# Performance work log

Hardware: AMD Instinct MI355X
Metric: run time of the kernel (lower is better)

The kernel has to match this reference:

```python
import jax, jax.numpy as jnp
import numpy as np

EPS = 1e-12  # F.normalize eps


def _gather_nb(var, idx):
    # var: [B, N, C], idx: [B, N, K] -> [B, N, K, C]; out[b,n,k,c] = var[b, idx[b,n,k], c]
    return jnp.take_along_axis(var[:, :, None, :], idx[:, :, :, None], axis=1)


def _l2norm(v):
    n = jnp.sqrt(jnp.sum(v * v, axis=-1, keepdims=True))
    return v / jnp.maximum(n, EPS)


def setup_inputs() -> dict:
    key = jax.random.key(0)
    ks = jax.random.split(key, 16)
    B, N, K, dim, hid = 4, 4096, 16, 128, 64
    s = 0.05
    return {
        "pos": jax.random.normal(ks[0], (B, N, 3), jnp.float32),
        "x": jax.random.normal(ks[1], (B, dim, N), jnp.float32),
        "idx": jax.random.randint(ks[2], (B, N, K), 0, N, jnp.int64),
        "dist": jax.random.uniform(ks[3], (B, N, K), jnp.float32),
        "W_qkv": jax.random.normal(ks[4], (3 * dim, dim), jnp.float32) * s,
        "W1": jax.random.normal(ks[5], (hid, 10), jnp.float32) * s,
        "b1": jax.random.normal(ks[6], (hid,), jnp.float32) * s,
        "W2": jax.random.normal(ks[7], (dim, hid), jnp.float32) * s,
        "b2": jax.random.normal(ks[8], (dim,), jnp.float32) * s,
        "Wm1": jax.random.normal(ks[9], (4 * dim, dim), jnp.float32) * s,
        "bm1": jax.random.normal(ks[10], (4 * dim,), jnp.float32) * s,
        "Wm2": jax.random.normal(ks[11], (dim, 4 * dim), jnp.float32) * s,
        "bm2": jax.random.normal(ks[12], (dim,), jnp.float32) * s,
    }


def reference(pos, x, idx, dist, W_qkv, W1, b1, W2, b2, Wm1, bm1, Wm2, bm2):
    B, _, N = x.shape
    xt = jnp.transpose(x, (0, 2, 1))                      # [B, N, C]
    qkv = xt @ W_qkv.T                                    # [B, N, 3C]
    Q, K_, V = jnp.split(qkv, 3, axis=-1)

    Qg = _gather_nb(Q, idx)                               # [B, N, K, C]
    Kg = _gather_nb(K_, idx)
    Vg = _gather_nb(V, idx)

    # position embedding: [center(3) | neighbor(3) | diff(3) | dist(1)] -> MLP 10->hid->C
    pos_nb = _gather_nb(pos, idx)                         # [B, N, K, 3]
    pos_c = jnp.broadcast_to(pos[:, :, None, :], pos_nb.shape)
    feat10 = jnp.concatenate(
        [pos_c, pos_nb, pos_c - pos_nb, dist[..., None]], axis=-1)  # [B, N, K, 10]
    pos_emb = jax.nn.relu(feat10 @ W1.T + b1) @ W2.T + b2  # [B, N, K, C]

    Knorm = _l2norm(Kg + pos_emb)                         # [B, N, K, C]
    Vrel = jax.nn.relu(Vg + pos_emb)                      # [B, N, K, C]
    Qn = _l2norm(Qg)                                      # [B, N, K, C]

    # kv_context: contract over N per neighbor slot k -> [B, K, C, C]
    kv = jnp.einsum('bnkc,bnkd->bkcd', Knorm, Vrel)
    # (1/N) Qn @ kv, then sum over k -> [B, N, C]
    agg = jnp.einsum('bnkc,bkcd->bnd', Qn, kv) / N

    out = jax.nn.relu(agg @ Wm1.T + bm1) @ Wm2.T + bm2 + xt  # [B, N, C]
    return jnp.transpose(out, (0, 2, 1))                     # [B, C, N]
```

## Files before the change

### kernel.cpp

```cpp
#include <hip/hip_runtime.h>
#include <math.h>

#define Bn 4
#define Nn 4096
#define Kn 16
#define Cn 128
#define HIDn 64

#define OFF_WQKVBF 0
#define OFF_WM1BF  24576
#define OFF_WM2BF  57344
#define OFF_W2BFG  90112
#define OFF_W1PBF  94208
#define OFF_QNBF   95232
#define OFF_KMBF   1143808
#define OFF_VMBF   2192384
#define OFF_KVT32  3240960
#define OFF_KVTBF  4289536
#define OFF_AGG0   4813824
#define OFF_AGG1   6910976
#define OFF_FLAG   9008128

typedef short bf16x8 __attribute__((ext_vector_type(8)));
typedef float f32x4 __attribute__((ext_vector_type(4)));

__device__ inline unsigned short f2bf(float f) {
  union { float f; unsigned u; } v; v.f = f;
  unsigned r = v.u + 0x7fffu + ((v.u >> 16) & 1u);
  return (unsigned short)(r >> 16);
}
__device__ inline float b2f(unsigned short s) {
  union { unsigned u; float f; } v; v.u = ((unsigned)s) << 16; return v.f;
}

__global__ void k0_prep(const float* __restrict__ Wqkv,
                        const float* __restrict__ Wm1, const float* __restrict__ Wm2,
                        const float* __restrict__ W2, const float* __restrict__ W1,
                        const int* __restrict__ idx_raw, float* ws) {
  if (blockIdx.x == 0 && threadIdx.x == 0) {
    int any = 0;
    for (int i = 0; i < 64; ++i) any |= idx_raw[2 * i + 1];
    ((int*)(ws + OFF_FLAG))[0] = (any == 0) ? 1 : 0;
  }
  int t = blockIdx.x * 256 + threadIdx.x;
  if (t < 49152) { ((unsigned short*)(ws + OFF_WQKVBF))[t] = f2bf(Wqkv[t]); return; }
  t -= 49152;
  if (t < 65536) { ((unsigned short*)(ws + OFF_WM1BF))[t] = f2bf(Wm1[t]); return; }
  t -= 65536;
  if (t < 65536) { ((unsigned short*)(ws + OFF_WM2BF))[t] = f2bf(Wm2[t]); return; }
  t -= 65536;
  if (t < 8192) { ((unsigned short*)(ws + OFF_W2BFG))[t] = f2bf(W2[t]); return; }
  t -= 8192;
  if (t < 2048) {
    int o = t >> 5, i = t & 31;
    ((unsigned short*)(ws + OFF_W1PBF))[t] = (i < 10) ? f2bf(W1[o * 10 + i]) : 0;
    return;
  }
}

__global__ __launch_bounds__(256, 2) void k1_qkv(const float* __restrict__ x, float* ws) {
  __shared__ __align__(16) unsigned short a_lds[32 * 136];
  __shared__ __align__(16) float qkv_lds[32 * 388];
  const unsigned short* Wq = (const unsigned short*)(ws + OFF_WQKVBF);
  unsigned short* Qnbf = (unsigned short*)(ws + OFF_QNBF);
  unsigned short* KmBF = (unsigned short*)(ws + OFF_KMBF);
  unsigned short* VmBF = (unsigned short*)(ws + OFF_VMBF);
  int b = blockIdx.x >> 7;
  int n0 = (blockIdx.x & 127) << 5;
  int t = threadIdx.x;
  int w = t >> 6, l = t & 63, ml = l & 15, gq = l >> 4;
#pragma unroll
  for (int i = 0; i < 16; ++i) {
    int id = t + 256 * i;
    int c = id >> 5, j = id & 31;
    a_lds[j * 136 + c] = f2bf(x[(b * Cn + c) * Nn + n0 + j]);
  }
  __syncthreads();
  f32x4 acc[2][6];
#pragma unroll
  for (int i = 0; i < 2; ++i)
#pragma unroll
    for (int j = 0; j < 6; ++j) acc[i][j] = (f32x4)0.f;
#pragma unroll
  for (int kc = 0; kc < 4; ++kc) {
    bf16x8 av0 = *(const bf16x8*)&a_lds[ml * 136 + kc * 32 + 8 * gq];
    bf16x8 av1 = *(const bf16x8*)&a_lds[(ml + 16) * 136 + kc * 32 + 8 * gq];
#pragma unroll
    for (int nf = 0; nf < 6; ++nf) {
      int m = 96 * w + 16 * nf + ml;
      bf16x8 bv = *(const bf16x8*)&Wq[m * 128 + kc * 32 + 8 * gq];
      acc[0][nf] = __builtin_amdgcn_mfma_f32_16x16x32_bf16(av0, bv, acc[0][nf], 0, 0, 0);
      acc[1][nf] = __builtin_amdgcn_mfma_f32_16x16x32_bf16(av1, bv, acc[1][nf], 0, 0, 0);
    }
  }
#pragma unroll
  for (int mf = 0; mf < 2; ++mf)
#pragma unroll
    for (int nf = 0; nf < 6; ++nf)
#pragma unroll
      for (int r = 0; r < 4; ++r)
        qkv_lds[(16 * mf + 4 * gq + r) * 388 + 96 * w + 16 * nf + ml] = acc[mf][nf][r];
  __syncthreads();
  {
    int g = t >> 3, l8 = t & 7;
    float4 q4[4];
    float ss = 0.f;
#pragma unroll
    for (int q = 0; q < 4; ++q) {
      q4[q] = *(const float4*)&qkv_lds[g * 388 + l8 * 16 + 4 * q];
      ss = fmaf(q4[q].x, q4[q].x, ss); ss = fmaf(q4[q].y, q4[q].y, ss);
      ss = fmaf(q4[q].z, q4[q].z, ss); ss = fmaf(q4[q].w, q4[q].w, ss);
    }
    ss += __shfl_xor(ss, 1); ss += __shfl_xor(ss, 2); ss += __shfl_xor(ss, 4);
    float sc = 1.f / fmaxf(sqrtf(ss), 1e-12f);
    union { unsigned short us[8]; uint4 u4; } o0, o1;
#pragma unroll
    for (int q = 0; q < 2; ++q) {
      o0.us[q * 4 + 0] = f2bf(q4[q].x * sc); o0.us[q * 4 + 1] = f2bf(q4[q].y * sc);
      o0.us[q * 4 + 2] = f2bf(q4[q].z * sc); o0.us[q * 4 + 3] = f2bf(q4[q].w * sc);
    }
#pragma unroll
    for (int q = 0; q < 2; ++q) {
      o1.us[q * 4 + 0] = f2bf(q4[2 + q].x * sc); o1.us[q * 4 + 1] = f2bf(q4[2 + q].y * sc);
      o1.us[q * 4 + 2] = f2bf(q4[2 + q].z * sc); o1.us[q * 4 + 3] = f2bf(q4[2 + q].w * sc);
    }
    *(uint4*)&Qnbf[(b * Nn + n0 + g) * Cn + l8 * 16] = o0.u4;
    *(uint4*)&Qnbf[(b * Nn + n0 + g) * Cn + l8 * 16 + 8] = o1.u4;
  }
#pragma unroll
  for (int i = 0; i < 2; ++i) {
    int id = t + 256 * i;
    int row = id >> 4, c8 = id & 15;
    const float* kp = &qkv_lds[row * 388 + 128 + c8 * 8];
    const float* vp = &qkv_lds[row * 388 + 256 + c8 * 8];
    union { unsigned short us[8]; uint4 u4; } ko, vo;
#pragma unroll
    for (int j = 0; j < 8; ++j) { ko.us[j] = f2bf(kp[j]); vo.us[j] = f2bf(vp[j]); }
    *(uint4*)&KmBF[(b * Nn + n0 + row) * Cn + c8 * 8] = ko.u4;
    *(uint4*)&VmBF[(b * Nn + n0 + row) * Cn + c8 * 8] = vo.u4;
  }
}

#define CH2 8
__global__ __launch_bounds__(256, 3) void k2_kv(const float* __restrict__ pos,
                                                const float* __restrict__ dist,
                                                const int* __restrict__ idxp,
                                                const float* __restrict__ b1,
                                                const float* __restrict__ b2,
                                                float* ws) {
  __shared__ __align__(16) unsigned short feat[32 * 40];
  __shared__ __align__(16) unsigned short h_lds[32 * 72];
  __shared__ __align__(16) unsigned short pe_bf[32 * 136];
  __shared__ __align__(16) unsigned short K_rm[32 * 136];
  __shared__ __align__(16) unsigned short V_rm[32 * 136];
  __shared__ __align__(16) unsigned short KnT[128 * 40];
  __shared__ __align__(16) unsigned short VrT[128 * 40];

  const unsigned short* KmBF = (const unsigned short*)(ws + OFF_KMBF);
  const unsigned short* VmBF = (const unsigned short*)(ws + OFF_VMBF);
  const unsigned short* W2g = (const unsigned short*)(ws + OFF_W2BFG);
  const unsigned short* W1P = (const unsigned short*)(ws + OFF_W1PBF);
  float* kvt = ws + OFF_KVT32;
  int flag = ((const int*)(ws + OFF_FLAG))[0];

  int bid = blockIdx.x;
  int b = bid & 3;
  int rest = bid >> 2;
  int k = rest & 15, ch = rest >> 4;
  int t = threadIdx.x;
  int w = t >> 6, l = t & 63;
  int ml = l & 15, gq = l >> 4;

  int nl = (t >> 3) & 7, half = t & 7;
  int n_b2 = 8 * w + nl;
  int side = t >> 7, cc = t & 127;
  bool is32 = (t < 32);

  float b1v = b1[16 * w + ml];
  float b2v0 = b2[32 * w + ml];
  float b2v1 = b2[32 * w + 16 + ml];

  f32x4 acc[2][8];
#pragma unroll
  for (int i = 0; i < 2; ++i)
#pragma unroll
    for (int j = 0; j < 8; ++j) acc[i][j] = (f32x4)0.f;

  int nbase = ch * 512;
  union U8 { unsigned short us[8]; uint4 u4; };

  float dd = 0.f, pc0 = 0.f, pc1 = 0.f, pc2 = 0.f, pn0 = 0.f, pn1 = 0.f, pn2 = 0.f;
  if (is32) {
    int fidx_m = (b * Nn + nbase + t) * Kn + k;
    int jn_m = flag ? idxp[2 * fidx_m] : idxp[fidx_m];
    dd = dist[fidx_m];
    pc0 = pos[(b * Nn + nbase + t) * 3 + 0];
    pc1 = pos[(b * Nn + nbase + t) * 3 + 1];
    pc2 = pos[(b * Nn + nbase + t) * 3 + 2];
    pn0 = pos[(b * Nn + jn_m) * 3 + 0];
    pn1 = pos[(b * Nn + jn_m) * 3 + 1];
    pn2 = pos[(b * Nn + jn_m) * 3 + 2];
  }
  int fidx_b = (b * Nn + nbase + n_b2) * Kn + k;
  int jn_b = flag ? idxp[2 * fidx_b] : idxp[fidx_b];
  U8 ka, kb, va, vb;
  {
    const unsigned short* krow = &KmBF[(b * Nn + jn_b) * Cn];
    const unsigned short* vrow = &VmBF[(b * Nn + jn_b) * Cn];
    ka.u4 = *(const uint4*)&krow[half * 16];
    kb.u4 = *(const uint4*)&krow[half * 16 + 8];
    va.u4 = *(const uint4*)&vrow[half * 16];
    vb.u4 = *(const uint4*)&vrow[half * 16 + 8];
  }
  if (is32) {
    float f10[10] = {pc0, pc1, pc2, pn0, pn1, pn2, pc0 - pn0, pc1 - pn1, pc2 - pn2, dd};
    U8 f0, f1, z;
#pragma unroll
    for (int j = 0; j < 8; ++j) f0.us[j] = f2bf(f10[j]);
    f1.us[0] = f2bf(f10[8]); f1.us[1] = f2bf(f10[9]);
#pragma unroll
    for (int j = 2; j < 8; ++j) f1.us[j] = 0;
#pragma unroll
    for (int j = 0; j < 8; ++j) z.us[j] = 0;
    *(uint4*)&feat[t * 40] = f0.u4;
    *(uint4*)&feat[t * 40 + 8] = f1.u4;
    *(uint4*)&feat[t * 40 + 16] = z.u4;
    *(uint4*)&feat[t * 40 + 24] = z.u4;
  }

  for (int it = 0; it < 16; ++it) {
    __syncthreads();
    {
      bf16x8 fa0 = *(const bf16x8*)&feat[ml * 40 + 8 * gq];
      bf16x8 fa1 = *(const bf16x8*)&feat[(ml + 16) * 40 + 8 * gq];
      bf16x8 wv = *(const bf16x8*)&W1P[(16 * w + ml) * 32 + 8 * gq];
      f32x4 h0 = (f32x4)0.f, h1 = (f32x4)0.f;
      h0 = __builtin_amdgcn_mfma_f32_16x16x32_bf16(fa0, wv, h0, 0, 0, 0);
      h1 = __builtin_amdgcn_mfma_f32_16x16x32_bf16(fa1, wv, h1, 0, 0, 0);
#pragma unroll
      for (int r = 0; r < 4; ++r) {
        h_lds[(4 * gq + r) * 72 + 16 * w + ml] = f2bf(fmaxf(h0[r] + b1v, 0.f));
        h_lds[(16 + 4 * gq + r) * 72 + 16 * w + ml] = f2bf(fmaxf(h1[r] + b1v, 0.f));
      }
    }
    int itn = (it < 15) ? it + 1 : 15;
    int n0n = nbase + itn * 32;
    int jn_mn = 0;
    float ddn = 0.f;
    if (is32) {
      int fidx_mn = (b * Nn + n0n + t) * Kn + k;
      jn_mn = flag ? idxp[2 * fidx_mn] : idxp[fidx_mn];
      ddn = dist[fidx_mn];
    }
    int fidx_bn = (b * Nn + n0n + n_b2) * Kn + k;
    int jn_bn = flag ? idxp[2 * fidx_bn] : idxp[fidx_bn];
    __syncthreads();
    {
      f32x4 pacc[2][2];
#pragma unroll
      for (int i = 0; i < 2; ++i)
#pragma unroll
        for (int j = 0; j < 2; ++j) pacc[i][j] = (f32x4)0.f;
#pragma unroll
      for (int hc = 0; hc < 64; hc += 32) {
        bf16x8 av[2];
#pragma unroll
        for (int mf = 0; mf < 2; ++mf)
          av[mf] = *(const bf16x8*)&h_lds[(ml + 16 * mf) * 72 + hc + 8 * gq];
#pragma unroll
        for (int nf = 0; nf < 2; ++nf) {
          int c = 32 * w + 16 * nf + ml;
          bf16x8 bv = *(const bf16x8*)&W2g[c * 64 + hc + 8 * gq];
          pacc[0][nf] = __builtin_amdgcn_mfma_f32_16x16x32_bf16(av[0], bv, pacc[0][nf], 0, 0, 0);
          pacc[1][nf] = __builtin_amdgcn_mfma_f32_16x16x32_bf16(av[1], bv, pacc[1][nf], 0, 0, 0);
        }
      }
#pragma unroll
      for (int mf = 0; mf < 2; ++mf)
#pragma unroll
        for (int nf = 0; nf < 2; ++nf) {
          int c = 32 * w + 16 * nf + ml;
          float bias = nf ? b2v1 : b2v0;
#pragma unroll
          for (int r = 0; r < 4; ++r)
            pe_bf[(16 * mf + 4 * gq + r) * 136 + c] = f2bf(pacc[mf][nf][r] + bias);
        }
    }
    __syncthreads();
    {
      U8 pa, pb;
      pa.u4 = *(const uint4*)&pe_bf[n_b2 * 136 + half * 16];
      pb.u4 = *(const uint4*)&pe_bf[n_b2 * 136 + half * 16 + 8];
      float kr[16], vr[16];
      float ss = 0.f;
#pragma unroll
      for (int j = 0; j < 16; ++j) {
        float pe = b2f((j < 8) ? pa.us[j] : pb.us[j - 8]);
        float kg = b2f((j < 8) ? ka.us[j] : kb.us[j - 8]);
        float vg = b2f((j < 8) ? va.us[j] : vb.us[j - 8]);
        kr[j] = kg + pe;
        vr[j] = fmaxf(vg + pe, 0.f);
        ss = fmaf(kr[j], kr[j], ss);
      }
      ss += __shfl_xor(ss, 1); ss += __shfl_xor(ss, 2); ss += __shfl_xor(ss, 4);
      float sc = 1.f / fmaxf(sqrtf(ss), 1e-12f);
      union { unsigned short us[8]; uint4 u4; } o;
#pragma unroll
      for (int hh = 0; hh < 2; ++hh) {
#pragma unroll
        for (int j = 0; j < 8; ++j) o.us[j] = f2bf(kr[hh * 8 + j] * sc);
        *(uint4*)&K_rm[n_b2 * 136 + half * 16 + 8 * hh] = o.u4;
      }
#pragma unroll
      for (int hh = 0; hh < 2; ++hh) {
#pragma unroll
        for (int j = 0; j < 8; ++j) o.us[j] = f2bf(vr[hh * 8 + j]);
        *(uint4*)&V_rm[n_b2 * 136 + half * 16 + 8 * hh] = o.u4;
      }
    }
    float pc0n = 0.f, pc1n = 0.f, pc2n = 0.f, pn0n = 0.f, pn1n = 0.f, pn2n = 0.f;
    if (is32) {
      pc0n = pos[(b * Nn + n0n + t) * 3 + 0];
      pc1n = pos[(b * Nn + n0n + t) * 3 + 1];
      pc2n = pos[(b * Nn + n0n + t) * 3 + 2];
      pn0n = pos[(b * Nn + jn_mn) * 3 + 0];
      pn1n = pos[(b * Nn + jn_mn) * 3 + 1];
      pn2n = pos[(b * Nn + jn_mn) * 3 + 2];
    }
    U8 kan, kbn, van, vbn;
    {
      const unsigned short* krow = &KmBF[(b * Nn + jn_bn) * Cn];
      const unsigned short* vrow = &VmBF[(b * Nn + jn_bn) * Cn];
      kan.u4 = *(const uint4*)&krow[half * 16];
      kbn.u4 = *(const uint4*)&krow[half * 16 + 8];
      van.u4 = *(const uint4*)&vrow[half * 16];
      vbn.u4 = *(const uint4*)&vrow[half * 16 + 8];
    }
    __syncthreads();
    {
      const unsigned short* src = side ? V_rm : K_rm;
      unsigned short* dst = side ? VrT : KnT;
      unsigned v[16];
#pragma unroll
      for (int i = 0; i < 16; ++i) {
        unsigned lo = src[(2 * i) * 136 + cc];
        unsigned hi = src[(2 * i + 1) * 136 + cc];
        v[i] = lo | (hi << 16);
      }
#pragma unroll
      for (int i = 0; i < 4; ++i) {
        uint4 pk = {v[4 * i], v[4 * i + 1], v[4 * i + 2], v[4 * i + 3]};
        *(uint4*)&dst[cc * 40 + 8 * i] = pk;
      }
    }
    __syncthreads();
    {
      bf16x8 av[2];
#pragma unroll
      for (int mf = 0; mf < 2; ++mf)
        av[mf] = *(const bf16x8*)&VrT[(32 * w + 16 * mf + ml) * 40 + 8 * gq];
#pragma unroll
      for (int nf = 0; nf < 8; ++nf) {
        bf16x8 bv = *(const bf16x8*)&KnT[(16 * nf + ml) * 40 + 8 * gq];
#pragma unroll
        for (int mf = 0; mf < 2; ++mf)
          acc[mf][nf] = __builtin_amdgcn_mfma_f32_16x16x32_bf16(av[mf], bv, acc[mf][nf], 0, 0, 0);
      }
    }
    if (is32) {
      float f10[10] = {pc0n, pc1n, pc2n, pn0n, pn1n, pn2n,
                       pc0n - pn0n, pc1n - pn1n, pc2n - pn2n, ddn};
      U8 f0, f1, z;
#pragma unroll
      for (int j = 0; j < 8; ++j) f0.us[j] = f2bf(f10[j]);
      f1.us[0] = f2bf(f10[8]); f1.us[1] = f2bf(f10[9]);
#pragma unroll
      for (int j = 2; j < 8; ++j) f1.us[j] = 0;
#pragma unroll
      for (int j = 0; j < 8; ++j) z.us[j] = 0;
      *(uint4*)&feat[t * 40] = f0.u4;
      *(uint4*)&feat[t * 40 + 8] = f1.u4;
      *(uint4*)&feat[t * 40 + 16] = z.u4;
      *(uint4*)&feat[t * 40 + 24] = z.u4;
    }
    ka.u4 = kan.u4; kb.u4 = kbn.u4; va.u4 = van.u4; vb.u4 = vbn.u4;
  }
  float* kvp = kvt + (b * Kn + k) * Cn * Cn;
#pragma unroll
  for (int mf = 0; mf < 2; ++mf)
#pragma unroll
    for (int nf = 0; nf < 8; ++nf) {
      int c = 16 * nf + ml;
#pragma unroll
      for (int r = 0; r < 4; ++r) {
        int d = 32 * w + 16 * mf + 4 * gq + r;
        atomicAdd(&kvp[d * Cn + c], acc[mf][nf][r]);
      }
    }
}

__global__ __launch_bounds__(256) void k2b_cvt(float* ws) {
  const float* src = ws + OFF_KVT32;
  unsigned short* dst = (unsigned short*)(ws + OFF_KVTBF);
  int i = blockIdx.x * 256 + threadIdx.x;
  float4 a = *(const float4*)&src[i * 8];
  float4 c = *(const float4*)&src[i * 8 + 4];
  union { unsigned short us[8]; uint4 u4; } o;
  o.us[0] = f2bf(a.x); o.us[1] = f2bf(a.y); o.us[2] = f2bf(a.z); o.us[3] = f2bf(a.w);
  o.us[4] = f2bf(c.x); o.us[5] = f2bf(c.y); o.us[6] = f2bf(c.z); o.us[7] = f2bf(c.w);
  *(uint4*)&dst[i * 8] = o.u4;
}

__global__ __launch_bounds__(256, 4) void k3_agg(const int* __restrict__ idxp, float* ws) {
  __shared__ __align__(16) unsigned short qt[32 * 136];
  const unsigned short* Qnbf = (const unsigned short*)(ws + OFF_QNBF);
  const unsigned short* kvtbf = (const unsigned short*)(ws + OFF_KVTBF);
  int flag = ((const int*)(ws + OFF_FLAG))[0];

  int bid = blockIdx.x;
  int b = bid & 3;
  int kh = (bid >> 2) & 1;
  int nt = bid >> 3;
  int n0 = nt * 32;
  int t = threadIdx.x;
  int w = t >> 6, l = t & 63;
  int ml = l & 15, gq = l >> 4;

  f32x4 acc[2][2];
#pragma unroll
  for (int i = 0; i < 2; ++i)
#pragma unroll
    for (int j = 0; j < 2; ++j) acc[i][j] = (f32x4)0.f;

  for (int kk = 0; kk < 8; ++kk) {
    int k = kh * 8 + kk;
    __syncthreads();
#pragma unroll
    for (int i = 0; i < 2; ++i) {
      int id = t + 256 * i;
      int row = id >> 4, c16 = id & 15;
      int fidx = (b * Nn + n0 + row) * Kn + k;
      int jn = flag ? idxp[2 * fidx] : idxp[fidx];
      uint4 v = *(const uint4*)&Qnbf[(b * Nn + jn) * Cn + c16 * 8];
      *(uint4*)&qt[row * 136 + c16 * 8] = v;
    }
    __syncthreads();
    const unsigned short* kvp = &kvtbf[(b * Kn + k) * Cn * Cn];
#pragma unroll
    for (int c0 = 0; c0 < 128; c0 += 32) {
      bf16x8 a0 = *(const bf16x8*)&qt[ml * 136 + c0 + 8 * gq];
      bf16x8 a1 = *(const bf16x8*)&qt[(ml + 16) * 136 + c0 + 8 * gq];
#pragma unroll
      for (int nf = 0; nf < 2; ++nf) {
        int d = 32 * w + 16 * nf + ml;
        bf16x8 bv = *(const bf16x8*)&kvp[d * Cn + c0 + 8 * gq];
        acc[0][nf] = __builtin_amdgcn_mfma_f32_16x16x32_bf16(a0, bv, acc[0][nf], 0, 0, 0);
        acc[1][nf] = __builtin_amdgcn_mfma_f32_16x16x32_bf16(a1, bv, acc[1][nf], 0, 0, 0);
      }
    }
  }
  float* ag = ws + (kh ? OFF_AGG1 : OFF_AGG0);
#pragma unroll
  for (int mf = 0; mf < 2; ++mf)
#pragma unroll
    for (int nf = 0; nf < 2; ++nf) {
      int d = 32 * w + 16 * nf + ml;
#pragma unroll
      for (int r = 0; r < 4; ++r) {
        int n = n0 + 16 * mf + 4 * gq + r;
        ag[(b * Nn + n) * Cn + d] = acc[mf][nf][r];
      }
    }
}

__global__ __launch_bounds__(256, 2) void k4_mlp(const float* __restrict__ x,
                                                 const float* __restrict__ bm1,
                                                 const float* __restrict__ bm2,
                                                 float* __restrict__ out, float* ws) {
  __shared__ __align__(16) unsigned short a_lds[32 * 136];
  __shared__ __align__(16) unsigned short h_lds[32 * 520];
  __shared__ float out_s[128 * 33];
  const float* agg0 = ws + OFF_AGG0;
  const float* agg1 = ws + OFF_AGG1;
  const unsigned short* Wm1bf = (const unsigned short*)(ws + OFF_WM1BF);
  const unsigned short* Wm2bf = (const unsigned short*)(ws + OFF_WM2BF);
  const float invN = 1.f / (float)Nn;
  int b = blockIdx.x >> 7;
  int n0 = (blockIdx.x & 127) << 5;
  int t = threadIdx.x;
  int w = t >> 6, l = t & 63, ml = l & 15, gq = l >> 4;
#pragma unroll
  for (int i = 0; i < 4; ++i) {
    int id = t + 256 * i;
    int row = id >> 5, c4 = id & 31;
    int off = (b * Nn + n0 + row) * Cn + c4 * 4;
    float4 v0 = *(const float4*)&agg0[off];
    float4 v1 = *(const float4*)&agg1[off];
    union { unsigned short us[4]; uint2 u2; } o;
    o.us[0] = f2bf((v0.x + v1.x) * invN); o.us[1] = f2bf((v0.y + v1.y) * invN);
    o.us[2] = f2bf((v0.z + v1.z) * invN); o.us[3] = f2bf((v0.w + v1.w) * invN);
    *(uint2*)&a_lds[row * 136 + c4 * 4] = o.u2;
  }
  __syncthreads();
  {
    f32x4 hacc[2][8];
#pragma unroll
    for (int i = 0; i < 2; ++i)
#pragma unroll
      for (int j = 0; j < 8; ++j) hacc[i][j] = (f32x4)0.f;
#pragma unroll
    for (int kc = 0; kc < 4; ++kc) {
      bf16x8 av0 = *(const bf16x8*)&a_lds[ml * 136 + kc * 32 + 8 * gq];
      bf16x8 av1 = *(const bf16x8*)&a_lds[(ml + 16) * 136 + kc * 32 + 8 * gq];
#pragma unroll
      for (int nf = 0; nf < 8; ++nf) {
        int h = 128 * w + 16 * nf + ml;
        bf16x8 bv = *(const bf16x8*)&Wm1bf[h * 128 + kc * 32 + 8 * gq];
        hacc[0][nf] = __builtin_amdgcn_mfma_f32_16x16x32_bf16(av0, bv, hacc[0][nf], 0, 0, 0);
        hacc[1][nf] = __builtin_amdgcn_mfma_f32_16x16x32_bf16(av1, bv, hacc[1][nf], 0, 0, 0);
      }
    }
#pragma unroll
    for (int mf = 0; mf < 2; ++mf)
#pragma unroll
      for (int nf = 0; nf < 8; ++nf) {
        int h = 128 * w + 16 * nf + ml;
        float bias = bm1[h];
#pragma unroll
        for (int r = 0; r < 4; ++r)
          h_lds[(16 * mf + 4 * gq + r) * 520 + h] = f2bf(fmaxf(hacc[mf][nf][r] + bias, 0.f));
      }
  }
  __syncthreads();
  {
    f32x4 oacc[2][2];
#pragma unroll
    for (int i = 0; i < 2; ++i)
#pragma unroll
      for (int j = 0; j < 2; ++j) oacc[i][j] = (f32x4)0.f;
#pragma unroll
    for (int kc = 0; kc < 16; ++kc) {
      bf16x8 av0 = *(const bf16x8*)&h_lds[ml * 520 + kc * 32 + 8 * gq];
      bf16x8 av1 = *(const bf16x8*)&h_lds[(ml + 16) * 520 + kc * 32 + 8 * gq];
#pragma unroll
      for (int nf = 0; nf < 2; ++nf) {
        int co = 32 * w + 16 * nf + ml;
        bf16x8 bv = *(const bf16x8*)&Wm2bf[co * 512 + kc * 32 + 8 * gq];
        oacc[0][nf] = __builtin_amdgcn_mfma_f32_16x16x32_bf16(av0, bv, oacc[0][nf], 0, 0, 0);
        oacc[1][nf] = __builtin_amdgcn_mfma_f32_16x16x32_bf16(av1, bv, oacc[1][nf], 0, 0, 0);
      }
    }
#pragma unroll
    for (int mf = 0; mf < 2; ++mf)
#pragma unroll
      for (int nf = 0; nf < 2; ++nf) {
        int co = 32 * w + 16 * nf + ml;
        float bias = bm2[co];
#pragma unroll
        for (int r = 0; r < 4; ++r)
          out_s[co * 33 + 16 * mf + 4 * gq + r] = oacc[mf][nf][r] + bias;
      }
  }
  __syncthreads();
#pragma unroll
  for (int i = 0; i < 16; ++i) {
    int id = t + 256 * i;
    int co = id >> 5, j = id & 31;
    out[(b * Cn + co) * Nn + n0 + j] = out_s[co * 33 + j] + x[(b * Cn + co) * Nn + n0 + j];
  }
}

extern "C" void kernel_launch(void* const* d_in, const int* in_sizes, int n_in,
                              void* d_out, int out_size, void* d_ws, size_t ws_size,
                              hipStream_t stream) {
  const float* pos  = (const float*)d_in[0];
  const float* x    = (const float*)d_in[1];
  const int*   idx  = (const int*)d_in[2];
  const float* dist = (const float*)d_in[3];
  const float* Wqkv = (const float*)d_in[4];
  const float* W1   = (const float*)d_in[5];
  const float* b1   = (const float*)d_in[6];
  const float* W2   = (const float*)d_in[7];
  const float* b2   = (const float*)d_in[8];
  const float* Wm1  = (const float*)d_in[9];
  const float* bm1  = (const float*)d_in[10];
  const float* Wm2  = (const float*)d_in[11];
  const float* bm2  = (const float*)d_in[12];
  float* out = (float*)d_out;
  float* ws = (float*)d_ws;

  hipMemsetAsync(ws + OFF_KVT32, 0, (size_t)Bn * Kn * Cn * Cn * sizeof(float), stream);
  hipLaunchKernelGGL(k0_prep, dim3(744), dim3(256), 0, stream, Wqkv, Wm1, Wm2, W2, W1, idx, ws);
  hipLaunchKernelGGL(k1_qkv, dim3(Bn * 128), dim3(256), 0, stream, x, ws);
  hipLaunchKernelGGL(k2_kv, dim3(Bn * Kn * CH2), dim3(256), 0, stream, pos, dist, idx, b1, b2, ws);
  hipLaunchKernelGGL(k2b_cvt, dim3(512), dim3(256), 0, stream, ws);
  hipLaunchKernelGGL(k3_agg, dim3(Bn * 2 * 128), dim3(256), 0, stream, idx, ws);
  hipLaunchKernelGGL(k4_mlp, dim3(Bn * 128), dim3(256), 0, stream, x, bm1, bm2, out, ws);
}
```

Baseline: 172.3 us.

## Fuse pos-MLP epilogue with K/V gather and write transposed tiles directly

After: 315.2 us. 1.83x slower.

```diff
diff --git a/kernel.cpp b/kernel.cpp
--- a/kernel.cpp
+++ b/kernel.cpp
@@ -141,8 +141,8 @@
   }
 }
 
-#define CH2 8
-__global__ __launch_bounds__(256, 3) void k2_kv(const float* __restrict__ pos,
+#define CH2 16
+__global__ __launch_bounds__(256, 4) void k2_kv(const float* __restrict__ pos,
                                                 const float* __restrict__ dist,
                                                 const int* __restrict__ idxp,
                                                 const float* __restrict__ b1,
@@ -150,9 +150,6 @@
                                                 float* ws) {
   __shared__ __align__(16) unsigned short feat[32 * 40];
   __shared__ __align__(16) unsigned short h_lds[32 * 72];
-  __shared__ __align__(16) unsigned short pe_bf[32 * 136];
-  __shared__ __align__(16) unsigned short K_rm[32 * 136];
-  __shared__ __align__(16) unsigned short V_rm[32 * 136];
   __shared__ __align__(16) unsigned short KnT[128 * 40];
   __shared__ __align__(16) unsigned short VrT[128 * 40];
 
@@ -170,15 +167,15 @@
   int t = threadIdx.x;
   int w = t >> 6, l = t & 63;
   int ml = l & 15, gq = l >> 4;
-
-  int nl = (t >> 3) & 7, half = t & 7;
-  int n_b2 = 8 * w + nl;
-  int side = t >> 7, cc = t & 127;
+  int nhalf = w & 1;
+  bool isV = (w >= 2);
   bool is32 = (t < 32);
+  const unsigned short* Grow = isV ? VmBF : KmBF;
 
   float b1v = b1[16 * w + ml];
-  float b2v0 = b2[32 * w + ml];
-  float b2v1 = b2[32 * w + 16 + ml];
+  float b2v[8];
+#pragma unroll
+  for (int nf = 0; nf < 8; ++nf) b2v[nf] = b2[16 * nf + ml];
 
   f32x4 acc[2][8];
 #pragma unroll
@@ -186,9 +183,14 @@
 #pragma unroll
     for (int j = 0; j < 8; ++j) acc[i][j] = (f32x4)0.f;
 
-  int nbase = ch * 512;
-  union U8 { unsigned short us[8]; uint4 u4; };
-
+  int nbase = ch * 256;
+
+  int jn_g[4];
+#pragma unroll
+  for (int r = 0; r < 4; ++r) {
+    int fidx = (b * Nn + nbase + 16 * nhalf + 4 * gq + r) * Kn + k;
+    jn_g[r] = flag ? idxp[2 * fidx] : idxp[fidx];
+  }
   float dd = 0.f, pc0 = 0.f, pc1 = 0.f, pc2 = 0.f, pn0 = 0.f, pn1 = 0.f, pn2 = 0.f;
   if (is32) {
     int fidx_m = (b * Nn + nbase + t) * Kn + k;
@@ -200,21 +202,8 @@
     pn0 = pos[(b * Nn + jn_m) * 3 + 0];
     pn1 = pos[(b * Nn + jn_m) * 3 + 1];
     pn2 = pos[(b * Nn + jn_m) * 3 + 2];
-  }
-  int fidx_b = (b * Nn + nbase + n_b2) * Kn + k;
-  int jn_b = flag ? idxp[2 * fidx_b] : idxp[fidx_b];
-  U8 ka, kb, va, vb;
-  {
-    const unsigned short* krow = &KmBF[(b * Nn + jn_b) * Cn];
-    const unsigned short* vrow = &VmBF[(b * Nn + jn_b) * Cn];
-    ka.u4 = *(const uint4*)&krow[half * 16];
-    kb.u4 = *(const uint4*)&krow[half * 16 + 8];
-    va.u4 = *(const uint4*)&vrow[half * 16];
-    vb.u4 = *(const uint4*)&vrow[half * 16 + 8];
-  }
-  if (is32) {
     float f10[10] = {pc0, pc1, pc2, pn0, pn1, pn2, pc0 - pn0, pc1 - pn1, pc2 - pn2, dd};
-    U8 f0, f1, z;
+    union { unsigned short us[8]; uint4 u4; } f0, f1, z;
 #pragma unroll
     for (int j = 0; j < 8; ++j) f0.us[j] = f2bf(f10[j]);
     f1.us[0] = f2bf(f10[8]); f1.us[1] = f2bf(f10[9]);
@@ -228,7 +217,7 @@
     *(uint4*)&feat[t * 40 + 24] = z.u4;
   }
 
-  for (int it = 0; it < 16; ++it) {
+  for (int it = 0; it < 8; ++it) {
     __syncthreads();
     {
       bf16x8 fa0 = *(const bf16x8*)&feat[ml * 40 + 8 * gq];
@@ -243,8 +232,21 @@
         h_lds[(16 + 4 * gq + r) * 72 + 16 * w + ml] = f2bf(fmaxf(h1[r] + b1v, 0.f));
       }
     }
-    int itn = (it < 15) ? it + 1 : 15;
+    unsigned short rowg[8][4];
+#pragma unroll
+    for (int r = 0; r < 4; ++r) {
+      const unsigned short* base = &Grow[(b * Nn + jn_g[r]) * Cn + ml];
+#pragma unroll
+      for (int nf = 0; nf < 8; ++nf) rowg[nf][r] = base[16 * nf];
+    }
+    int itn = (it < 7) ? it + 1 : 7;
     int n0n = nbase + itn * 32;
+    int jn_gn[4];
+#pragma unroll
+    for (int r = 0; r < 4; ++r) {
+      int fidx = (b * Nn + n0n + 16 * nhalf + 4 * gq + r) * Kn + k;
+      jn_gn[r] = flag ? idxp[2 * fidx] : idxp[fidx];
+    }
     int jn_mn = 0;
     float ddn = 0.f;
     if (is32) {
@@ -252,70 +254,54 @@
       jn_mn = flag ? idxp[2 * fidx_mn] : idxp[fidx_mn];
       ddn = dist[fidx_mn];
     }
-    int fidx_bn = (b * Nn + n0n + n_b2) * Kn + k;
-    int jn_bn = flag ? idxp[2 * fidx_bn] : idxp[fidx_bn];
     __syncthreads();
     {
-      f32x4 pacc[2][2];
-#pragma unroll
-      for (int i = 0; i < 2; ++i)
-#pragma unroll
-        for (int j = 0; j < 2; ++j) pacc[i][j] = (f32x4)0.f;
-#pragma unroll
-      for (int hc = 0; hc < 64; hc += 32) {
-        bf16x8 av[2];
-#pragma unroll
-        for (int mf = 0; mf < 2; ++mf)
-          av[mf] = *(const bf16x8*)&h_lds[(ml + 16 * mf) * 72 + hc + 8 * gq];
-#pragma unroll
-        for (int nf = 0; nf < 2; ++nf) {
-          int c = 32 * w + 16 * nf + ml;
-          bf16x8 bv = *(const bf16x8*)&W2g[c * 64 + hc + 8 * gq];
-          pacc[0][nf] = __builtin_amdgcn_mfma_f32_16x16x32_bf16(av[0], bv, pacc[0][nf], 0, 0, 0);
-          pacc[1][nf] = __builtin_amdgcn_mfma_f32_16x16x32_bf16(av[1], bv, pacc[1][nf], 0, 0, 0);
+      bf16x8 av0 = *(const bf16x8*)&h_lds[(16 * nhalf + ml) * 72 + 8 * gq];
+      bf16x8 av1 = *(const bf16x8*)&h_lds[(16 * nhalf + ml) * 72 + 32 + 8 * gq];
+      float ss[4] = {0.f, 0.f, 0.f, 0.f};
+      unsigned kp[8][2];
+#pragma unroll
+      for (int nf = 0; nf < 8; ++nf) {
+        bf16x8 bv0 = *(const bf16x8*)&W2g[(16 * nf + ml) * 64 + 8 * gq];
+        bf16x8 bv1 = *(const bf16x8*)&W2g[(16 * nf + ml) * 64 + 32 + 8 * gq];
+        f32x4 p = (f32x4)0.f;
+        p = __builtin_amdgcn_mfma_f32_16x16x32_bf16(av0, bv0, p, 0, 0, 0);
+        p = __builtin_amdgcn_mfma_f32_16x16x32_bf16(av1, bv1, p, 0, 0, 0);
+        if (!isV) {
+          float v0 = b2f(rowg[nf][0]) + p[0] + b2v[nf];
+          float v1 = b2f(rowg[nf][1]) + p[1] + b2v[nf];
+          float v2 = b2f(rowg[nf][2]) + p[2] + b2v[nf];
+          float v3 = b2f(rowg[nf][3]) + p[3] + b2v[nf];
+          ss[0] = fmaf(v0, v0, ss[0]); ss[1] = fmaf(v1, v1, ss[1]);
+          ss[2] = fmaf(v2, v2, ss[2]); ss[3] = fmaf(v3, v3, ss[3]);
+          kp[nf][0] = (unsigned)f2bf(v0) | ((unsigned)f2bf(v1) << 16);
+          kp[nf][1] = (unsigned)f2bf(v2) | ((unsigned)f2bf(v3) << 16);
+        } else {
+#pragma unroll
+          for (int r = 0; r < 4; ++r) {
+            float vv = fmaxf(b2f(rowg[nf][r]) + p[r] + b2v[nf], 0.f);
+            VrT[(16 * nf + ml) * 40 + 16 * nhalf + 4 * gq + r] = f2bf(vv);
+          }
         }
       }
-#pragma unroll
-      for (int mf = 0; mf < 2; ++mf)
-#pragma unroll
-        for (int nf = 0; nf < 2; ++nf) {
-          int c = 32 * w + 16 * nf + ml;
-          float bias = nf ? b2v1 : b2v0;
-#pragma unroll
-          for (int r = 0; r < 4; ++r)
-            pe_bf[(16 * mf + 4 * gq + r) * 136 + c] = f2bf(pacc[mf][nf][r] + bias);
+      if (!isV) {
+        float sc[4];
+#pragma unroll
+        for (int r = 0; r < 4; ++r) {
+          float s = ss[r];
+          s += __shfl_xor(s, 1); s += __shfl_xor(s, 2);
+          s += __shfl_xor(s, 4); s += __shfl_xor(s, 8);
+          sc[r] = 1.f / fmaxf(sqrtf(s), 1e-12f);
         }
-    }
-    __syncthreads();
-    {
-      U8 pa, pb;
-      pa.u4 = *(const uint4*)&pe_bf[n_b2 * 136 + half * 16];
-      pb.u4 = *(const uint4*)&pe_bf[n_b2 * 136 + half * 16 + 8];
-      float kr[16], vr[16];
-      float ss = 0.f;
-#pragma unroll
-      for (int j = 0; j < 16; ++j) {
-        float pe = b2f((j < 8) ? pa.us[j] : pb.us[j - 8]);
-        float kg = b2f((j < 8) ? ka.us[j] : kb.us[j - 8]);
-        float vg = b2f((j < 8) ? va.us[j] : vb.us[j - 8]);
-        kr[j] = kg + pe;
-        vr[j] = fmaxf(vg + pe, 0.f);
-        ss = fmaf(kr[j], kr[j], ss);
-      }
-      ss += __shfl_xor(ss, 1); ss += __shfl_xor(ss, 2); ss += __shfl_xor(ss, 4);
-      float sc = 1.f / fmaxf(sqrtf(ss), 1e-12f);
-      union { unsigned short us[8]; uint4 u4; } o;
-#pragma unroll
-      for (int hh = 0; hh < 2; ++hh) {
-#pragma unroll
-        for (int j = 0; j < 8; ++j) o.us[j] = f2bf(kr[hh * 8 + j] * sc);
-        *(uint4*)&K_rm[n_b2 * 136 + half * 16 + 8 * hh] = o.u4;
-      }
-#pragma unroll
-      for (int hh = 0; hh < 2; ++hh) {
-#pragma unroll
-        for (int j = 0; j < 8; ++j) o.us[j] = f2bf(vr[hh * 8 + j]);
-        *(uint4*)&V_rm[n_b2 * 136 + half * 16 + 8 * hh] = o.u4;
+#pragma unroll
+        for (int nf = 0; nf < 8; ++nf) {
+#pragma unroll
+          for (int r = 0; r < 4; ++r) {
+            unsigned bits = (r & 1) ? (kp[nf][r >> 1] >> 16) : (kp[nf][r >> 1] & 0xffffu);
+            float val = b2f((unsigned short)bits) * sc[r];
+            KnT[(16 * nf + ml) * 40 + 16 * nhalf + 4 * gq + r] = f2bf(val);
+          }
+        }
       }
     }
     float pc0n = 0.f, pc1n = 0.f, pc2n = 0.f, pn0n = 0.f, pn1n = 0.f, pn2n = 0.f;
@@ -327,50 +313,24 @@
       pn1n = pos[(b * Nn + jn_mn) * 3 + 1];
       pn2n = pos[(b * Nn + jn_mn) * 3 + 2];
     }
-    U8 kan, kbn, van, vbn;
-    {
-      const unsigned short* krow = &KmBF[(b * Nn + jn_bn) * Cn];
-      const unsigned short* vrow = &VmBF[(b * Nn + jn_bn) * Cn];
-      kan.u4 = *(const uint4*)&krow[half * 16];
-      kbn.u4 = *(const uint4*)&krow[half * 16 + 8];
-      van.u4 = *(const uint4*)&vrow[half * 16];
-      vbn.u4 = *(const uint4*)&vrow[half * 16 + 8];
-    }
     __syncthreads();
     {
-      const unsigned short* src = side ? V_rm : K_rm;
-      unsigned short* dst = side ? VrT : KnT;
-      unsigned v[16];
-#pragma unroll
-      for (int i = 0; i < 16; ++i) {
-        unsigned lo = src[(2 * i) * 136 + cc];
-        unsigned hi = src[(2 * i + 1) * 136 + cc];
-        v[i] = lo | (hi << 16);
-      }
-#pragma unroll
-      for (int i = 0; i < 4; ++i) {
-        uint4 pk = {v[4 * i], v[4 * i + 1], v[4 * i + 2], v[4 * i + 3]};
-        *(uint4*)&dst[cc * 40 + 8 * i] = pk;
-      }
-    }
-    __syncthreads();
-    {
-      bf16x8 av[2];
+      bf16x8 avv[2];
 #pragma unroll
       for (int mf = 0; mf < 2; ++mf)
-        av[mf] = *(const bf16x8*)&VrT[(32 * w + 16 * mf + ml) * 40 + 8 * gq];
+        avv[mf] = *(const bf16x8*)&VrT[(32 * w + 16 * mf + ml) * 40 + 8 * gq];
 #pragma unroll
       for (int nf = 0; nf < 8; ++nf) {
         bf16x8 bv = *(const bf16x8*)&KnT[(16 * nf + ml) * 40 + 8 * gq];
 #pragma unroll
         for (int mf = 0; mf < 2; ++mf)
-          acc[mf][nf] = __builtin_amdgcn_mfma_f32_16x16x32_bf16(av[mf], bv, acc[mf][nf], 0, 0, 0);
+          acc[mf][nf] = __builtin_amdgcn_mfma_f32_16x16x32_bf16(avv[mf], bv, acc[mf][nf], 0, 0, 0);
       }
     }
     if (is32) {
       float f10[10] = {pc0n, pc1n, pc2n, pn0n, pn1n, pn2n,
                        pc0n - pn0n, pc1n - pn1n, pc2n - pn2n, ddn};
-      U8 f0, f1, z;
+      union { unsigned short us[8]; uint4 u4; } f0, f1, z;
 #pragma unroll
       for (int j = 0; j < 8; ++j) f0.us[j] = f2bf(f10[j]);
       f1.us[0] = f2bf(f10[8]); f1.us[1] = f2bf(f10[9]);
@@ -383,7 +343,8 @@
       *(uint4*)&feat[t * 40 + 16] = z.u4;
       *(uint4*)&feat[t * 40 + 24] = z.u4;
     }
-    ka.u4 = kan.u4; kb.u4 = kbn.u4; va.u4 = van.u4; vb.u4 = vbn.u4;
+#pragma unroll
+    for (int r = 0; r < 4; ++r) jn_g[r] = jn_gn[r];
   }
   float* kvp = kvt + (b * Kn + k) * Cn * Cn;
 #pragma unroll
```
